# Optimization experiments

Hardware: AMD Instinct MI355X
Metric: run time of the kernel (lower is better)

The kernel has to match this reference:

```python
import jax, jax.numpy as jnp
from jax import lax
import numpy as np

N_LAYER = 2
SEQ, BATCH, D = 4096, 32, 512


def setup_inputs() -> dict:
    key = jax.random.key(0)
    k1, k2, k3 = jax.random.split(key, 3)
    x = jax.random.normal(k1, (SEQ, BATCH, D), dtype=jnp.float32)
    # repo init: weight_ih ~ N(0, 0.01)
    W_ih = jax.random.normal(k2, (N_LAYER, D, D), dtype=jnp.float32) * 0.01
    # recurrent weight in [0,1) keeps the long ReLU recurrence bounded
    w_hh = jax.random.uniform(k3, (N_LAYER, D), dtype=jnp.float32)
    b_ih = jnp.zeros((N_LAYER, D), dtype=jnp.float32)
    return {"x": x, "W_ih": W_ih, "w_hh": w_hh, "b_ih": b_ih}


def _indrnn_layer(x, W, w, b):
    # x: (T, B, in), W: (H, in), w,b: (H,)
    proj = jnp.einsum('tbi,hi->tbh', x, W) + b  # one batched GEMM up front

    def step(h, p):
        h = jax.nn.relu(p + w * h)
        return h, h

    h0 = jnp.zeros((x.shape[1], W.shape[0]), dtype=x.dtype)
    hT, ys = lax.scan(step, h0, proj)
    return ys, hT


def reference(x, W_ih, w_hh, b_ih):
    hiddens = []
    out = x
    for l in range(W_ih.shape[0]):  # small fixed layer loop
        out, hT = _indrnn_layer(out, W_ih[l], w_hh[l], b_ih[l])
        hiddens.append(hT)
    h_n = jnp.stack(hiddens, axis=0)  # (n_layer, B, H)
    return out, h_n
```

## Files before the change

kernel.cpp:

```cpp
#include <hip/hip_runtime.h>

#define T_SEQ   4096
#define BATCH   32
#define DIM     512
#define MROWS   (T_SEQ * BATCH)
#define S_STRIDE (BATCH * DIM)
#define OUT_ELEMS ((size_t)T_SEQ * BATCH * DIM)
#define NCH     32
#define CLEN    (T_SEQ / NCH)
#define NCHAIN  (BATCH * DIM)
#define NWG     ((MROWS / 128) * (DIM / 128))

typedef __bf16 bf8_t __attribute__((ext_vector_type(8)));
typedef float  f4_t  __attribute__((ext_vector_type(4)));
typedef unsigned short u16x8 __attribute__((ext_vector_type(8)));
typedef __attribute__((address_space(1))) void gvoid_t;
typedef __attribute__((address_space(3))) void lvoid_t;

__device__ __forceinline__ unsigned short f2bf(float f) {
    unsigned int u = __float_as_uint(f);
    u += 0x7FFFu + ((u >> 16) & 1u);
    return (unsigned short)(u >> 16);
}
__device__ __forceinline__ float bf2f(unsigned short b) {
    return __uint_as_float(((unsigned int)b) << 16);
}

__global__ __launch_bounds__(256) void k_cvt(const float* __restrict__ in,
                                             unsigned short* __restrict__ out) {
    size_t i = ((size_t)blockIdx.x * 256 + threadIdx.x) * 8;
    float4 a = *reinterpret_cast<const float4*>(in + i);
    float4 b = *reinterpret_cast<const float4*>(in + i + 4);
    u16x8 o;
    o[0] = f2bf(a.x); o[1] = f2bf(a.y); o[2] = f2bf(a.z); o[3] = f2bf(a.w);
    o[4] = f2bf(b.x); o[5] = f2bf(b.y); o[6] = f2bf(b.z); o[7] = f2bf(b.w);
    *reinterpret_cast<u16x8*>(out + i) = o;
}

template <int AF32>
__global__ __launch_bounds__(256)
void k_gemm_bt(const void* __restrict__ Ap,
               const unsigned short* __restrict__ B,
               unsigned short* __restrict__ C) {
    __shared__ unsigned short As[128 * 32];
    __shared__ unsigned short Bs[128 * 32];

    const int tid  = threadIdx.x;
    const int lane = tid & 63;
    const int wv   = tid >> 6;
    const int wr   = wv >> 1;
    const int wc   = wv & 1;

    const int flat = blockIdx.x;
    const int s    = (flat & 7) * (NWG / 8) + (flat >> 3);
    const size_t gm = (size_t)(s >> 2) * 128;
    const int    gn = (s & 3) * 128;

    const int srow = tid >> 2;
    const int skk  = (tid & 3) * 8;

    f4_t acc[4][4] = {};

    const int l15 = lane & 15;
    const int lk  = (lane >> 4) * 8;

    for (int k0 = 0; k0 < 512; k0 += 32) {
#pragma unroll
        for (int i = 0; i < 2; ++i) {
            const unsigned short* gb = B + (size_t)(gn + i * 64 + srow) * 512 + k0 + skk;
            __builtin_amdgcn_global_load_lds((gvoid_t*)gb, (lvoid_t*)&Bs[i * 2048 + wv * 512], 16, 0, 0);
            if constexpr (AF32) {
                const float* ga = (const float*)Ap + (gm + (size_t)(i * 64 + srow)) * 512 + k0 + skk;
                float4 a0 = *reinterpret_cast<const float4*>(ga);
                float4 a1 = *reinterpret_cast<const float4*>(ga + 4);
                u16x8 o;
                o[0] = f2bf(a0.x); o[1] = f2bf(a0.y); o[2] = f2bf(a0.z); o[3] = f2bf(a0.w);
                o[4] = f2bf(a1.x); o[5] = f2bf(a1.y); o[6] = f2bf(a1.z); o[7] = f2bf(a1.w);
                *reinterpret_cast<u16x8*>(&As[i * 2048 + tid * 8]) = o;
            } else {
                const unsigned short* ga = (const unsigned short*)Ap + (gm + (size_t)(i * 64 + srow)) * 512 + k0 + skk;
                __builtin_amdgcn_global_load_lds((gvoid_t*)ga, (lvoid_t*)&As[i * 2048 + wv * 512], 16, 0, 0);
            }
        }
        __syncthreads();

        bf8_t af[4], bfz[4];
#pragma unroll
        for (int m = 0; m < 4; ++m)
            af[m] = *reinterpret_cast<const bf8_t*>(&As[(wr * 64 + m * 16 + l15) * 32 + lk]);
#pragma unroll
        for (int n = 0; n < 4; ++n)
            bfz[n] = *reinterpret_cast<const bf8_t*>(&Bs[(wc * 64 + n * 16 + l15) * 32 + lk]);
#pragma unroll
        for (int m = 0; m < 4; ++m)
#pragma unroll
            for (int n = 0; n < 4; ++n)
                acc[m][n] = __builtin_amdgcn_mfma_f32_16x16x32_bf16(af[m], bfz[n], acc[m][n], 0, 0, 0);
        __syncthreads();
    }

    const int crow0 = (lane >> 4) * 4;
#pragma unroll
    for (int m = 0; m < 4; ++m)
#pragma unroll
        for (int n = 0; n < 4; ++n) {
            const size_t row0 = gm + (size_t)(wr * 64 + m * 16 + crow0);
            const int    col  = gn + wc * 64 + n * 16 + l15;
#pragma unroll
            for (int r = 0; r < 4; ++r)
                C[(row0 + r) * 512 + col] = f2bf(acc[m][n][r]);
        }
}

__global__ __launch_bounds__(256)
void k_scan_p1(const unsigned short* __restrict__ q,
               const float* __restrict__ w_hh,
               const float* __restrict__ b_ih,
               float* __restrict__ Asum,
               float* __restrict__ Bsum) {
    const int g = (blockIdx.x & 63) * 256 + threadIdx.x;
    const int c = blockIdx.x >> 6;
    const float w  = w_hh[g & 511];
    const float bs = b_ih[g & 511];
    const unsigned short* p = q + (size_t)c * CLEN * S_STRIDE + g;

    float A = 0.f, Bv = 0.f;
    float s0[8], s1[8];
#pragma unroll
    for (int j = 0; j < 8; ++j) s0[j] = bf2f(p[(size_t)j * S_STRIDE]);
#pragma unroll
    for (int j = 0; j < 8; ++j) s1[j] = bf2f(p[(size_t)(8 + j) * S_STRIDE]);

    for (int j0 = 0; j0 < CLEN; j0 += 16) {
#pragma unroll
        for (int j = 0; j < 8; ++j) {
            float qv = s0[j] + bs;
            A  = fmaxf(fmaf(w, A, qv), 0.f);
            Bv = fmaf(w, Bv, qv);
        }
        if (j0 + 16 < CLEN) {
#pragma unroll
            for (int j = 0; j < 8; ++j) s0[j] = bf2f(p[(size_t)(j0 + 16 + j) * S_STRIDE]);
        }
#pragma unroll
        for (int j = 0; j < 8; ++j) {
            float qv = s1[j] + bs;
            A  = fmaxf(fmaf(w, A, qv), 0.f);
            Bv = fmaf(w, Bv, qv);
        }
        if (j0 + 24 < CLEN) {
#pragma unroll
            for (int j = 0; j < 8; ++j) s1[j] = bf2f(p[(size_t)(j0 + 24 + j) * S_STRIDE]);
        }
    }
    Asum[(size_t)c * NCHAIN + g] = A;
    Bsum[(size_t)c * NCHAIN + g] = Bv;
}

template <int MODE>
__global__ __launch_bounds__(256)
void k_scan_p2(const unsigned short* __restrict__ q,
               const float* __restrict__ w_hh,
               const float* __restrict__ b_ih,
               const float* __restrict__ Asum,
               const float* __restrict__ Bsum,
               float* __restrict__ of32,
               unsigned short* __restrict__ ob16,
               float* __restrict__ hT) {
    const int g = (blockIdx.x & 63) * 256 + threadIdx.x;
    const int c = blockIdx.x >> 6;
    const float w  = w_hh[g & 511];
    const float bs = b_ih[g & 511];

    float cw = w;
#pragma unroll
    for (int i = 0; i < 7; ++i) cw *= cw;
    float h = 0.f;
    for (int cc = 0; cc < c; ++cc)
        h = fmaxf(Asum[(size_t)cc * NCHAIN + g], fmaf(cw, h, Bsum[(size_t)cc * NCHAIN + g]));

    const size_t base = (size_t)c * CLEN * S_STRIDE + g;
    const unsigned short* p = q + base;

    float s0[8], s1[8];
#pragma unroll
    for (int j = 0; j < 8; ++j) s0[j] = bf2f(p[(size_t)j * S_STRIDE]);
#pragma unroll
    for (int j = 0; j < 8; ++j) s1[j] = bf2f(p[(size_t)(8 + j) * S_STRIDE]);

    for (int j0 = 0; j0 < CLEN; j0 += 16) {
#pragma unroll
        for (int j = 0; j < 8; ++j) {
            h = fmaxf(fmaf(w, h, s0[j] + bs), 0.f);
            const size_t idx = base + (size_t)(j0 + j) * S_STRIDE;
            if (MODE == 0) of32[idx] = h; else ob16[idx] = f2bf(h);
        }
        if (j0 + 16 < CLEN) {
#pragma unroll
            for (int j = 0; j < 8; ++j) s0[j] = bf2f(p[(size_t)(j0 + 16 + j) * S_STRIDE]);
        }
#pragma unroll
        for (int j = 0; j < 8; ++j) {
            h = fmaxf(fmaf(w, h, s1[j] + bs), 0.f);
            const size_t idx = base + (size_t)(j0 + 8 + j) * S_STRIDE;
            if (MODE == 0) of32[idx] = h; else ob16[idx] = f2bf(h);
        }
        if (j0 + 24 < CLEN) {
#pragma unroll
            for (int j = 0; j < 8; ++j) s1[j] = bf2f(p[(size_t)(j0 + 24 + j) * S_STRIDE]);
        }
    }
    if (c == NCH - 1) hT[g] = h;
}

extern "C" void kernel_launch(void* const* d_in, const int* in_sizes, int n_in,
                              void* d_out, int out_size, void* d_ws, size_t ws_size,
                              hipStream_t stream) {
    const float* x    = (const float*)d_in[0];
    const float* W_ih = (const float*)d_in[1];
    const float* w_hh = (const float*)d_in[2];
    const float* b_ih = (const float*)d_in[3];

    unsigned short* proj2 = (unsigned short*)d_ws;
    unsigned short* Wb    = proj2 + OUT_ELEMS;
    float* Asum = (float*)(Wb + 2 * 512 * 512);
    float* Bsum = Asum + (size_t)NCH * NCHAIN;

    unsigned short* proj1 = (unsigned short*)d_out;
    unsigned short* ys1   = proj1 + OUT_ELEMS;
    float* out = (float*)d_out;
    float* hT  = out + OUT_ELEMS;

    const int sgrid = 64 * NCH;

    k_cvt<<<524288 / 8 / 256, 256, 0, stream>>>(W_ih, Wb);
    k_gemm_bt<1><<<NWG, 256, 0, stream>>>(x, Wb, proj1);
    k_scan_p1<<<sgrid, 256, 0, stream>>>(proj1, w_hh, b_ih, Asum, Bsum);
    k_scan_p2<1><<<sgrid, 256, 0, stream>>>(proj1, w_hh, b_ih, Asum, Bsum,
                                            nullptr, ys1, hT);
    k_gemm_bt<0><<<NWG, 256, 0, stream>>>(ys1, Wb + 512 * 512, proj2);
    k_scan_p1<<<sgrid, 256, 0, stream>>>(proj2, w_hh + DIM, b_ih + DIM, Asum, Bsum);
    k_scan_p2<0><<<sgrid, 256, 0, stream>>>(proj2, w_hh + DIM, b_ih + DIM, Asum, Bsum,
                                            out, nullptr, hT + NCHAIN);
}
```

Before: 469.1 us.

## Rewrite projection GEMM to keep full weight slice resident in LDS

The tiled GEMM, which staged both A and B through LDS in K-steps of 32 with two barriers per step, is replaced. Each workgroup now loads a full 128x512 weight slice (padded rows) into LDS once. Its eight waves then stream A rows straight from global memory into registers, with software-pipelined prefetch, across 2048 rows. This removes per-K-step barriers and A staging through LDS and reuses B across many row tiles. In exchange it uses about 130KB of dynamic LDS per block, direct uncoalesced-ish per-lane A loads, a 256-block grid, and heavy register pressure at 512 threads with a min-blocks-per-CU hint of 2.

```diff
diff --git a/kernel.cpp b/kernel.cpp
--- a/kernel.cpp
+++ b/kernel.cpp
@@ -9,13 +9,13 @@
 #define NCH     32
 #define CLEN    (T_SEQ / NCH)
 #define NCHAIN  (BATCH * DIM)
-#define NWG     ((MROWS / 128) * (DIM / 128))
+
+#define BROW    520
+#define LDS_BYTES (128 * BROW * 2)
 
 typedef __bf16 bf8_t __attribute__((ext_vector_type(8)));
 typedef float  f4_t  __attribute__((ext_vector_type(4)));
 typedef unsigned short u16x8 __attribute__((ext_vector_type(8)));
-typedef __attribute__((address_space(1))) void gvoid_t;
-typedef __attribute__((address_space(3))) void lvoid_t;
 
 __device__ __forceinline__ unsigned short f2bf(float f) {
     unsigned int u = __float_as_uint(f);
@@ -38,78 +38,102 @@
 }
 
 template <int AF32>
-__global__ __launch_bounds__(256)
-void k_gemm_bt(const void* __restrict__ Ap,
+__global__ __launch_bounds__(512, 2)
+void k_gemm_rs(const void* __restrict__ Ap,
                const unsigned short* __restrict__ B,
                unsigned short* __restrict__ C) {
-    __shared__ unsigned short As[128 * 32];
-    __shared__ unsigned short Bs[128 * 32];
+    extern __shared__ unsigned short Bs[];
 
     const int tid  = threadIdx.x;
     const int lane = tid & 63;
-    const int wv   = tid >> 6;
-    const int wr   = wv >> 1;
-    const int wc   = wv & 1;
-
-    const int flat = blockIdx.x;
-    const int s    = (flat & 7) * (NWG / 8) + (flat >> 3);
-    const size_t gm = (size_t)(s >> 2) * 128;
-    const int    gn = (s & 3) * 128;
-
-    const int srow = tid >> 2;
-    const int skk  = (tid & 3) * 8;
-
-    f4_t acc[4][4] = {};
-
-    const int l15 = lane & 15;
-    const int lk  = (lane >> 4) * 8;
-
-    for (int k0 = 0; k0 < 512; k0 += 32) {
-#pragma unroll
-        for (int i = 0; i < 2; ++i) {
-            const unsigned short* gb = B + (size_t)(gn + i * 64 + srow) * 512 + k0 + skk;
-            __builtin_amdgcn_global_load_lds((gvoid_t*)gb, (lvoid_t*)&Bs[i * 2048 + wv * 512], 16, 0, 0);
-            if constexpr (AF32) {
-                const float* ga = (const float*)Ap + (gm + (size_t)(i * 64 + srow)) * 512 + k0 + skk;
-                float4 a0 = *reinterpret_cast<const float4*>(ga);
-                float4 a1 = *reinterpret_cast<const float4*>(ga + 4);
-                u16x8 o;
-                o[0] = f2bf(a0.x); o[1] = f2bf(a0.y); o[2] = f2bf(a0.z); o[3] = f2bf(a0.w);
-                o[4] = f2bf(a1.x); o[5] = f2bf(a1.y); o[6] = f2bf(a1.z); o[7] = f2bf(a1.w);
-                *reinterpret_cast<u16x8*>(&As[i * 2048 + tid * 8]) = o;
-            } else {
-                const unsigned short* ga = (const unsigned short*)Ap + (gm + (size_t)(i * 64 + srow)) * 512 + k0 + skk;
-                __builtin_amdgcn_global_load_lds((gvoid_t*)ga, (lvoid_t*)&As[i * 2048 + wv * 512], 16, 0, 0);
+    const int w    = tid >> 6;
+    const int l15  = lane & 15;
+    const int lk   = (lane >> 4) * 8;
+    const int n_t  = blockIdx.x >> 6;
+    const int mg   = blockIdx.x & 63;
+    const int gn   = n_t * 128;
+
+    {
+        const int lc = tid >> 2, s0 = tid & 3;
+        const unsigned short* gB = B + (size_t)(gn + lc) * 512;
+#pragma unroll
+        for (int j = 0; j < 16; ++j) {
+            const int seg = j * 4 + s0;
+            u16x8 v = *reinterpret_cast<const u16x8*>(gB + seg * 8);
+            *reinterpret_cast<u16x8*>(&Bs[lc * BROW + seg * 8]) = v;
+        }
+    }
+    __syncthreads();
+
+    const int bbase = l15 * BROW + lk;
+
+    for (int ms = 0; ms < 8; ++ms) {
+        const size_t R0 = (size_t)mg * 2048 + ms * 256 + w * 32;
+        f4_t acc[2][8] = {};
+
+        const unsigned short* arp[2];
+        const float*          afp[2];
+#pragma unroll
+        for (int m = 0; m < 2; ++m) {
+            if constexpr (AF32) afp[m] = (const float*)Ap + (R0 + m * 16 + l15) * 512;
+            else                arp[m] = (const unsigned short*)Ap + (R0 + m * 16 + l15) * 512;
+        }
+
+        bf8_t a0[2], a1[2], a2[2], b0[8], b1[8];
+
+#define LOAD_A(dst, k0)                                                        \
+        _Pragma("unroll")                                                      \
+        for (int m = 0; m < 2; ++m) {                                          \
+            if constexpr (AF32) {                                              \
+                float4 f0 = *reinterpret_cast<const float4*>(afp[m] + (k0) + lk);     \
+                float4 f1 = *reinterpret_cast<const float4*>(afp[m] + (k0) + lk + 4); \
+                u16x8 o;                                                       \
+                o[0] = f2bf(f0.x); o[1] = f2bf(f0.y); o[2] = f2bf(f0.z); o[3] = f2bf(f0.w); \
+                o[4] = f2bf(f1.x); o[5] = f2bf(f1.y); o[6] = f2bf(f1.z); o[7] = f2bf(f1.w); \
+                dst[m] = *reinterpret_cast<bf8_t*>(&o);                        \
+            } else {                                                           \
+                dst[m] = *reinterpret_cast<const bf8_t*>(arp[m] + (k0) + lk);  \
+            }                                                                  \
+        }
+#define LOAD_B(dst, k0)                                                        \
+        _Pragma("unroll")                                                      \
+        for (int n = 0; n < 8; ++n)                                            \
+            dst[n] = *reinterpret_cast<const bf8_t*>(&Bs[bbase + n * 16 * BROW + (k0)]);
+
+        LOAD_A(a0, 0)
+        LOAD_A(a1, 32)
+        LOAD_B(b0, 0)
+
+#pragma unroll
+        for (int ks = 0; ks < 16; ++ks) {
+            const int k0 = ks * 32;
+            if (ks < 14) { LOAD_A(a2, k0 + 64) }
+            if (ks < 15) { LOAD_B(b1, k0 + 32) }
+#pragma unroll
+            for (int m = 0; m < 2; ++m)
+#pragma unroll
+                for (int n = 0; n < 8; ++n)
+                    acc[m][n] = __builtin_amdgcn_mfma_f32_16x16x32_bf16(a0[m], b0[n], acc[m][n], 0, 0, 0);
+#pragma unroll
+            for (int m = 0; m < 2; ++m) { a0[m] = a1[m]; a1[m] = a2[m]; }
+#pragma unroll
+            for (int n = 0; n < 8; ++n) b0[n] = b1[n];
+        }
+#undef LOAD_A
+#undef LOAD_B
+
+        const int crow0 = (lane >> 4) * 4;
+#pragma unroll
+        for (int m = 0; m < 2; ++m)
+#pragma unroll
+            for (int n = 0; n < 8; ++n) {
+                const size_t row0 = R0 + m * 16 + crow0;
+                const int    col  = gn + n * 16 + l15;
+#pragma unroll
+                for (int r = 0; r < 4; ++r)
+                    C[(row0 + r) * 512 + col] = f2bf(acc[m][n][r]);
             }
-        }
-        __syncthreads();
-
-        bf8_t af[4], bfz[4];
-#pragma unroll
-        for (int m = 0; m < 4; ++m)
-            af[m] = *reinterpret_cast<const bf8_t*>(&As[(wr * 64 + m * 16 + l15) * 32 + lk]);
-#pragma unroll
-        for (int n = 0; n < 4; ++n)
-            bfz[n] = *reinterpret_cast<const bf8_t*>(&Bs[(wc * 64 + n * 16 + l15) * 32 + lk]);
-#pragma unroll
-        for (int m = 0; m < 4; ++m)
-#pragma unroll
-            for (int n = 0; n < 4; ++n)
-                acc[m][n] = __builtin_amdgcn_mfma_f32_16x16x32_bf16(af[m], bfz[n], acc[m][n], 0, 0, 0);
-        __syncthreads();
-    }
-
-    const int crow0 = (lane >> 4) * 4;
-#pragma unroll
-    for (int m = 0; m < 4; ++m)
-#pragma unroll
-        for (int n = 0; n < 4; ++n) {
-            const size_t row0 = gm + (size_t)(wr * 64 + m * 16 + crow0);
-            const int    col  = gn + wc * 64 + n * 16 + l15;
-#pragma unroll
-            for (int r = 0; r < 4; ++r)
-                C[(row0 + r) * 512 + col] = f2bf(acc[m][n][r]);
-        }
+    }
 }
 
 __global__ __launch_bounds__(256)
@@ -234,11 +258,11 @@
     const int sgrid = 64 * NCH;
 
     k_cvt<<<524288 / 8 / 256, 256, 0, stream>>>(W_ih, Wb);
-    k_gemm_bt<1><<<NWG, 256, 0, stream>>>(x, Wb, proj1);
+    k_gemm_rs<1><<<256, 512, LDS_BYTES, stream>>>(x, Wb, proj1);
     k_scan_p1<<<sgrid, 256, 0, stream>>>(proj1, w_hh, b_ih, Asum, Bsum);
     k_scan_p2<1><<<sgrid, 256, 0, stream>>>(proj1, w_hh, b_ih, Asum, Bsum,
                                             nullptr, ys1, hT);
-    k_gemm_bt<0><<<NWG, 256, 0, stream>>>(ys1, Wb + 512 * 512, proj2);
+    k_gemm_rs<0><<<256, 512, LDS_BYTES, stream>>>(ys1, Wb + 512 * 512, proj2);
     k_scan_p1<<<sgrid, 256, 0, stream>>>(proj2, w_hh + DIM, b_ih + DIM, Asum, Bsum);
     k_scan_p2<0><<<sgrid, 256, 0, stream>>>(proj2, w_hh + DIM, b_ih + DIM, Asum, Bsum,
                                             out, nullptr, hT + NCHAIN);
```

Result: slower. 1.139 ms (+142.9%).

## Double-buffer LDS tiles in bf16 GEMM to overlap loads with MFMA

Applied to the files above, without the earlier changes.

Splits the GEMM's LDS A/B tiles into two buffers and prefetches the next K-slice (async global_load_lds for bf16, register-staged float loads for the f32 A path) while MFMAs run on the current slice. This drops one __syncthreads per K-iteration and is meant to hide global memory latency behind compute. In exchange it doubles LDS use per workgroup, which may reduce occupancy, and the f32 path holds extra registers for the staged loads.

```diff
diff --git a/kernel.cpp b/kernel.cpp
--- a/kernel.cpp
+++ b/kernel.cpp
@@ -42,8 +42,8 @@
 void k_gemm_bt(const void* __restrict__ Ap,
                const unsigned short* __restrict__ B,
                unsigned short* __restrict__ C) {
-    __shared__ unsigned short As[128 * 32];
-    __shared__ unsigned short Bs[128 * 32];
+    __shared__ unsigned short As[2][128 * 32];
+    __shared__ unsigned short Bs[2][128 * 32];
 
     const int tid  = threadIdx.x;
     const int lane = tid & 63;
@@ -60,44 +60,77 @@
     const int skk  = (tid & 3) * 8;
 
     f4_t acc[4][4] = {};
-
     const int l15 = lane & 15;
     const int lk  = (lane >> 4) * 8;
 
-    for (int k0 = 0; k0 < 512; k0 += 32) {
-#pragma unroll
-        for (int i = 0; i < 2; ++i) {
-            const unsigned short* gb = B + (size_t)(gn + i * 64 + srow) * 512 + k0 + skk;
-            __builtin_amdgcn_global_load_lds((gvoid_t*)gb, (lvoid_t*)&Bs[i * 2048 + wv * 512], 16, 0, 0);
-            if constexpr (AF32) {
-                const float* ga = (const float*)Ap + (gm + (size_t)(i * 64 + srow)) * 512 + k0 + skk;
-                float4 a0 = *reinterpret_cast<const float4*>(ga);
-                float4 a1 = *reinterpret_cast<const float4*>(ga + 4);
-                u16x8 o;
-                o[0] = f2bf(a0.x); o[1] = f2bf(a0.y); o[2] = f2bf(a0.z); o[3] = f2bf(a0.w);
-                o[4] = f2bf(a1.x); o[5] = f2bf(a1.y); o[6] = f2bf(a1.z); o[7] = f2bf(a1.w);
-                *reinterpret_cast<u16x8*>(&As[i * 2048 + tid * 8]) = o;
-            } else {
-                const unsigned short* ga = (const unsigned short*)Ap + (gm + (size_t)(i * 64 + srow)) * 512 + k0 + skk;
-                __builtin_amdgcn_global_load_lds((gvoid_t*)ga, (lvoid_t*)&As[i * 2048 + wv * 512], 16, 0, 0);
-            }
-        }
-        __syncthreads();
+    float4 fa0[2], fa1[2];
+
+#define ISSUE_A_F32(k0)                                                        \
+    _Pragma("unroll")                                                          \
+    for (int i = 0; i < 2; ++i) {                                              \
+        const float* ga = (const float*)Ap + (gm + (size_t)(i * 64 + srow)) * 512 + (k0) + skk; \
+        fa0[i] = *reinterpret_cast<const float4*>(ga);                         \
+        fa1[i] = *reinterpret_cast<const float4*>(ga + 4);                     \
+    }
+#define WRITE_A_F32(b)                                                         \
+    _Pragma("unroll")                                                          \
+    for (int i = 0; i < 2; ++i) {                                              \
+        u16x8 o;                                                               \
+        o[0] = f2bf(fa0[i].x); o[1] = f2bf(fa0[i].y); o[2] = f2bf(fa0[i].z); o[3] = f2bf(fa0[i].w); \
+        o[4] = f2bf(fa1[i].x); o[5] = f2bf(fa1[i].y); o[6] = f2bf(fa1[i].z); o[7] = f2bf(fa1[i].w); \
+        *reinterpret_cast<u16x8*>(&As[b][i * 2048 + tid * 8]) = o;             \
+    }
+#define GLL_A(b, k0)                                                           \
+    _Pragma("unroll")                                                          \
+    for (int i = 0; i < 2; ++i) {                                              \
+        const unsigned short* ga = (const unsigned short*)Ap + (gm + (size_t)(i * 64 + srow)) * 512 + (k0) + skk; \
+        __builtin_amdgcn_global_load_lds((gvoid_t*)ga, (lvoid_t*)&As[b][i * 2048 + wv * 512], 16, 0, 0); \
+    }
+#define GLL_B(b, k0)                                                           \
+    _Pragma("unroll")                                                          \
+    for (int i = 0; i < 2; ++i) {                                              \
+        const unsigned short* gb = B + (size_t)(gn + i * 64 + srow) * 512 + (k0) + skk; \
+        __builtin_amdgcn_global_load_lds((gvoid_t*)gb, (lvoid_t*)&Bs[b][i * 2048 + wv * 512], 16, 0, 0); \
+    }
+
+    if constexpr (AF32) { ISSUE_A_F32(0) } else { GLL_A(0, 0) }
+    GLL_B(0, 0)
+    if constexpr (AF32) { WRITE_A_F32(0) }
+    __syncthreads();
+
+#pragma unroll 2
+    for (int ks = 0; ks < 16; ++ks) {
+        const int cur = ks & 1;
+        const int nxt = cur ^ 1;
+        const int k1  = (ks + 1) * 32;
+
+        if (ks < 15) {
+            if constexpr (AF32) { ISSUE_A_F32(k1) } else { GLL_A(nxt, k1) }
+            GLL_B(nxt, k1)
+        }
 
         bf8_t af[4], bfz[4];
 #pragma unroll
         for (int m = 0; m < 4; ++m)
-            af[m] = *reinterpret_cast<const bf8_t*>(&As[(wr * 64 + m * 16 + l15) * 32 + lk]);
+            af[m] = *reinterpret_cast<const bf8_t*>(&As[cur][(wr * 64 + m * 16 + l15) * 32 + lk]);
 #pragma unroll
         for (int n = 0; n < 4; ++n)
-            bfz[n] = *reinterpret_cast<const bf8_t*>(&Bs[(wc * 64 + n * 16 + l15) * 32 + lk]);
+            bfz[n] = *reinterpret_cast<const bf8_t*>(&Bs[cur][(wc * 64 + n * 16 + l15) * 32 + lk]);
 #pragma unroll
         for (int m = 0; m < 4; ++m)
 #pragma unroll
             for (int n = 0; n < 4; ++n)
                 acc[m][n] = __builtin_amdgcn_mfma_f32_16x16x32_bf16(af[m], bfz[n], acc[m][n], 0, 0, 0);
+
+        if (ks < 15) {
+            if constexpr (AF32) { WRITE_A_F32(nxt) }
+        }
         __syncthreads();
     }
+#undef ISSUE_A_F32
+#undef WRITE_A_F32
+#undef GLL_A
+#undef GLL_B
 
     const int crow0 = (lane >> 4) * 4;
 #pragma unroll
```

Measured after the change: 465.8 us. No clear change (-0.7%).

## Rewrite projection GEMM as 256x256 double-buffered 8-wave pipelined kernel

Applied to the files above, without the earlier changes.

Replaces the 128x128, 4-wave, single-buffered GEMM with a 256x256-tile, 8-wave kernel. It uses a 64-wide K step, double-buffered LDS with an XOR swizzle, and explicit waitcnt/barrier/setprio phases so global loads overlap MFMA work. For the fp32 input layer, the A tile is prefetched into registers and converted to bf16 while the previous tile computes. The cost is about 128KB of dynamic LDS per block and far fewer workgroups. This lowers occupancy, and the hand-counted vmcnt scheduling can break silently if the load counts change.

```diff
diff --git a/kernel.cpp b/kernel.cpp
--- a/kernel.cpp
+++ b/kernel.cpp
@@ -9,7 +9,13 @@
 #define NCH     32
 #define CLEN    (T_SEQ / NCH)
 #define NCHAIN  (BATCH * DIM)
-#define NWG     ((MROWS / 128) * (DIM / 128))
+
+#define GNWG    ((MROWS / 256) * (DIM / 256))
+#define OFF_A0  0
+#define OFF_A1  16384
+#define OFF_B0  32768
+#define OFF_B1  49152
+#define GLDS_B  131072
 
 typedef __bf16 bf8_t __attribute__((ext_vector_type(8)));
 typedef float  f4_t  __attribute__((ext_vector_type(4)));
@@ -25,6 +31,15 @@
 __device__ __forceinline__ float bf2f(unsigned short b) {
     return __uint_as_float(((unsigned int)b) << 16);
 }
+
+#define VMC(n)  asm volatile("s_waitcnt vmcnt(" #n ")" ::: "memory")
+#define LGKM0   asm volatile("s_waitcnt lgkmcnt(0)" ::: "memory")
+#define PH_PRE()  do { __builtin_amdgcn_s_barrier(); LGKM0;                    \
+                       __builtin_amdgcn_sched_barrier(0);                      \
+                       __builtin_amdgcn_s_setprio(1); } while (0)
+#define PH_POST() do { __builtin_amdgcn_s_setprio(0);                          \
+                       __builtin_amdgcn_sched_barrier(0);                      \
+                       __builtin_amdgcn_s_barrier(); } while (0)
 
 __global__ __launch_bounds__(256) void k_cvt(const float* __restrict__ in,
                                              unsigned short* __restrict__ out) {
@@ -38,73 +53,177 @@
 }
 
 template <int AF32>
-__global__ __launch_bounds__(256)
-void k_gemm_bt(const void* __restrict__ Ap,
-               const unsigned short* __restrict__ B,
-               unsigned short* __restrict__ C) {
-    __shared__ unsigned short As[128 * 32];
-    __shared__ unsigned short Bs[128 * 32];
+__global__ __launch_bounds__(512, 2)
+void k_gemm8(const void* __restrict__ Ap,
+             const unsigned short* __restrict__ Bp,
+             unsigned short* __restrict__ C) {
+    extern __shared__ unsigned short lds[];
 
     const int tid  = threadIdx.x;
     const int lane = tid & 63;
     const int wv   = tid >> 6;
-    const int wr   = wv >> 1;
-    const int wc   = wv & 1;
-
-    const int flat = blockIdx.x;
-    const int s    = (flat & 7) * (NWG / 8) + (flat >> 3);
-    const size_t gm = (size_t)(s >> 2) * 128;
-    const int    gn = (s & 3) * 128;
-
-    const int srow = tid >> 2;
-    const int skk  = (tid & 3) * 8;
-
-    f4_t acc[4][4] = {};
-
-    const int l15 = lane & 15;
-    const int lk  = (lane >> 4) * 8;
-
-    for (int k0 = 0; k0 < 512; k0 += 32) {
-#pragma unroll
-        for (int i = 0; i < 2; ++i) {
-            const unsigned short* gb = B + (size_t)(gn + i * 64 + srow) * 512 + k0 + skk;
-            __builtin_amdgcn_global_load_lds((gvoid_t*)gb, (lvoid_t*)&Bs[i * 2048 + wv * 512], 16, 0, 0);
-            if constexpr (AF32) {
-                const float* ga = (const float*)Ap + (gm + (size_t)(i * 64 + srow)) * 512 + k0 + skk;
-                float4 a0 = *reinterpret_cast<const float4*>(ga);
-                float4 a1 = *reinterpret_cast<const float4*>(ga + 4);
-                u16x8 o;
-                o[0] = f2bf(a0.x); o[1] = f2bf(a0.y); o[2] = f2bf(a0.z); o[3] = f2bf(a0.w);
-                o[4] = f2bf(a1.x); o[5] = f2bf(a1.y); o[6] = f2bf(a1.z); o[7] = f2bf(a1.w);
-                *reinterpret_cast<u16x8*>(&As[i * 2048 + tid * 8]) = o;
-            } else {
-                const unsigned short* ga = (const unsigned short*)Ap + (gm + (size_t)(i * 64 + srow)) * 512 + k0 + skk;
-                __builtin_amdgcn_global_load_lds((gvoid_t*)ga, (lvoid_t*)&As[i * 2048 + wv * 512], 16, 0, 0);
+    const int wr   = wv >> 2;
+    const int wc   = wv & 3;
+    const int l15  = lane & 15;
+    const int l16  = lane >> 4;
+    const int lj   = lane >> 3;
+    const int ss8  = lane & 7;
+
+    const int sid = (blockIdx.x & 7) * (GNWG / 8) + (blockIdx.x >> 3);
+    const size_t gm = (size_t)(sid >> 1) * 256;
+    const int    gn = (sid & 1) * 256;
+
+    const unsigned short* Ab = (const unsigned short*)Ap;
+    const float*          Af = (const float*)Ap;
+
+    auto stage = [&](const unsigned short* gbase, size_t grow0, int region,
+                     int half, int kt) {
+#pragma unroll
+        for (int j = 0; j < 2; ++j) {
+            const int r = half * 128 + j * 64 + wv * 8 + lj;
+            const unsigned short* src =
+                gbase + (grow0 + r) * 512 + kt * 64 + ((ss8 ^ (r & 7)) * 8);
+            unsigned short* dst = &lds[region + half * 8192 + j * 4096 + wv * 512];
+            __builtin_amdgcn_global_load_lds((gvoid_t*)src, (lvoid_t*)dst, 16, 0, 0);
+        }
+    };
+    auto loadAf = [&](float4* h, int half, int kt) {
+#pragma unroll
+        for (int j = 0; j < 2; ++j) {
+            const int r = half * 128 + j * 64 + wv * 8 + lj;
+            const float* src = Af + (gm + r) * 512 + kt * 64 + ss8 * 8;
+            h[j * 2]     = *reinterpret_cast<const float4*>(src);
+            h[j * 2 + 1] = *reinterpret_cast<const float4*>(src + 4);
+        }
+    };
+    auto writeAf = [&](const float4* h, int region, int half) {
+#pragma unroll
+        for (int j = 0; j < 2; ++j) {
+            const int r = half * 128 + j * 64 + wv * 8 + lj;
+            float4 f0 = h[j * 2], f1 = h[j * 2 + 1];
+            u16x8 o;
+            o[0] = f2bf(f0.x); o[1] = f2bf(f0.y); o[2] = f2bf(f0.z); o[3] = f2bf(f0.w);
+            o[4] = f2bf(f1.x); o[5] = f2bf(f1.y); o[6] = f2bf(f1.z); o[7] = f2bf(f1.w);
+            *reinterpret_cast<u16x8*>(&lds[region + r * 64 + (ss8 ^ (r & 7)) * 8]) = o;
+        }
+    };
+
+    f4_t  acc[8][4] = {};
+    bf8_t bb[4][2];
+    bf8_t aq[2][2];
+    float4 afh0[4], afh1[4];
+
+    auto loadBall = [&](int region) {
+#pragma unroll
+        for (int n = 0; n < 4; ++n)
+#pragma unroll
+            for (int ks = 0; ks < 2; ++ks) {
+                const int c  = wc * 64 + n * 16 + l15;
+                const int sl = (ks * 4 + l16) ^ (l15 & 7);
+                bb[n][ks] = *reinterpret_cast<const bf8_t*>(
+                    (const char*)&lds[region] + c * 128 + sl * 16);
             }
-        }
-        __syncthreads();
-
-        bf8_t af[4], bfz[4];
-#pragma unroll
-        for (int m = 0; m < 4; ++m)
-            af[m] = *reinterpret_cast<const bf8_t*>(&As[(wr * 64 + m * 16 + l15) * 32 + lk]);
-#pragma unroll
-        for (int n = 0; n < 4; ++n)
-            bfz[n] = *reinterpret_cast<const bf8_t*>(&Bs[(wc * 64 + n * 16 + l15) * 32 + lk]);
-#pragma unroll
-        for (int m = 0; m < 4; ++m)
-#pragma unroll
-            for (int n = 0; n < 4; ++n)
-                acc[m][n] = __builtin_amdgcn_mfma_f32_16x16x32_bf16(af[m], bfz[n], acc[m][n], 0, 0, 0);
-        __syncthreads();
+    };
+    auto loadAq = [&](int region, int q) {
+#pragma unroll
+        for (int m = 0; m < 2; ++m)
+#pragma unroll
+            for (int ks = 0; ks < 2; ++ks) {
+                const int r  = wr * 128 + (q * 2 + m) * 16 + l15;
+                const int sl = (ks * 4 + l16) ^ (l15 & 7);
+                aq[m][ks] = *reinterpret_cast<const bf8_t*>(
+                    (const char*)&lds[region] + r * 128 + sl * 16);
+            }
+    };
+#define MFMA_Q(q)                                                              \
+    _Pragma("unroll")                                                          \
+    for (int m = 0; m < 2; ++m)                                                \
+        _Pragma("unroll")                                                      \
+        for (int n = 0; n < 4; ++n)                                            \
+            _Pragma("unroll")                                                  \
+            for (int ks = 0; ks < 2; ++ks)                                     \
+                acc[(q) * 2 + m][n] = __builtin_amdgcn_mfma_f32_16x16x32_bf16( \
+                    aq[m][ks], bb[n][ks], acc[(q) * 2 + m][n], 0, 0, 0);
+
+    if constexpr (AF32) {
+        loadAf(afh0, 0, 0); loadAf(afh1, 1, 0);
+        stage(Bp, (size_t)gn, OFF_B0, 0, 0); stage(Bp, (size_t)gn, OFF_B0, 1, 0);
+        stage(Bp, (size_t)gn, OFF_B1, 0, 1); stage(Bp, (size_t)gn, OFF_B1, 1, 1);
+        VMC(8);
+        writeAf(afh0, OFF_A0, 0); writeAf(afh1, OFF_A0, 1);
+        VMC(4);
+        LGKM0;
+    } else {
+        stage(Ab, gm, OFF_A0, 0, 0); stage(Ab, gm, OFF_A0, 1, 0);
+        stage(Bp, (size_t)gn, OFF_B0, 0, 0); stage(Bp, (size_t)gn, OFF_B0, 1, 0);
+        stage(Bp, (size_t)gn, OFF_B1, 0, 1); stage(Bp, (size_t)gn, OFF_B1, 1, 1);
+        VMC(4);
     }
-
-    const int crow0 = (lane >> 4) * 4;
-#pragma unroll
-    for (int m = 0; m < 4; ++m)
+    __builtin_amdgcn_s_barrier();
+
+#pragma unroll
+    for (int i = 0; i < 4; ++i) {
+        const int t1 = 2 * i + 1, t2 = 2 * i + 2, t3 = 2 * i + 3;
+        const bool st2 = (i < 3);
+
+        loadBall(OFF_B0); loadAq(OFF_A0, 0);
+        if constexpr (AF32) { loadAf(afh0, 0, t1); } else { stage(Ab, gm, OFF_A1, 0, t1); }
+        PH_PRE(); MFMA_Q(0); PH_POST();
+        loadAq(OFF_A0, 1);
+        if constexpr (AF32) { loadAf(afh1, 1, t1); } else { stage(Ab, gm, OFF_A1, 1, t1); }
+        PH_PRE(); MFMA_Q(1); PH_POST();
+        loadAq(OFF_A0, 2);
+        if (st2) stage(Bp, (size_t)gn, OFF_B0, 0, t2);
+        PH_PRE(); MFMA_Q(2);
+        __builtin_amdgcn_s_setprio(0); __builtin_amdgcn_sched_barrier(0);
+        if constexpr (AF32) {
+            if (st2) { VMC(6); } else { VMC(4); }
+            writeAf(afh0, OFF_A1, 0);
+        }
+        __builtin_amdgcn_s_barrier();
+        loadAq(OFF_A0, 3);
+        if (st2) stage(Bp, (size_t)gn, OFF_B0, 1, t2);
+        PH_PRE(); MFMA_Q(3);
+        __builtin_amdgcn_s_setprio(0); __builtin_amdgcn_sched_barrier(0);
+        if constexpr (AF32) {
+            if (st2) { VMC(4); } else { VMC(0); }
+            writeAf(afh1, OFF_A1, 1);
+            LGKM0;
+        } else {
+            if (st2) { VMC(4); } else { VMC(0); }
+        }
+        __builtin_amdgcn_s_barrier();
+
+        loadBall(OFF_B1); loadAq(OFF_A1, 0);
+        if (st2) { if constexpr (AF32) { loadAf(afh0, 0, t2); } else { stage(Ab, gm, OFF_A0, 0, t2); } }
+        PH_PRE(); MFMA_Q(0); PH_POST();
+        loadAq(OFF_A1, 1);
+        if (st2) { if constexpr (AF32) { loadAf(afh1, 1, t2); } else { stage(Ab, gm, OFF_A0, 1, t2); } }
+        PH_PRE(); MFMA_Q(1); PH_POST();
+        loadAq(OFF_A1, 2);
+        if (st2) stage(Bp, (size_t)gn, OFF_B1, 0, t3);
+        PH_PRE(); MFMA_Q(2);
+        __builtin_amdgcn_s_setprio(0); __builtin_amdgcn_sched_barrier(0);
+        if constexpr (AF32) { if (st2) { VMC(6); writeAf(afh0, OFF_A0, 0); } }
+        __builtin_amdgcn_s_barrier();
+        loadAq(OFF_A1, 3);
+        if (st2) stage(Bp, (size_t)gn, OFF_B1, 1, t3);
+        PH_PRE(); MFMA_Q(3);
+        __builtin_amdgcn_s_setprio(0); __builtin_amdgcn_sched_barrier(0);
+        if (st2) {
+            VMC(4);
+            if constexpr (AF32) { writeAf(afh1, OFF_A0, 1); LGKM0; }
+        }
+        __builtin_amdgcn_s_barrier();
+    }
+#undef MFMA_Q
+
+    const int crow0 = l16 * 4;
+#pragma unroll
+    for (int m = 0; m < 8; ++m)
 #pragma unroll
         for (int n = 0; n < 4; ++n) {
-            const size_t row0 = gm + (size_t)(wr * 64 + m * 16 + crow0);
+            const size_t row0 = gm + (size_t)(wr * 128 + m * 16 + crow0);
             const int    col  = gn + wc * 64 + n * 16 + l15;
 #pragma unroll
             for (int r = 0; r < 4; ++r)
@@ -221,6 +340,11 @@
     const float* w_hh = (const float*)d_in[2];
     const float* b_ih = (const float*)d_in[3];
 
+    hipFuncSetAttribute(reinterpret_cast<const void*>(&k_gemm8<1>),
+                        hipFuncAttributeMaxDynamicSharedMemorySize, GLDS_B);
+    hipFuncSetAttribute(reinterpret_cast<const void*>(&k_gemm8<0>),
+                        hipFuncAttributeMaxDynamicSharedMemorySize, GLDS_B);
+
     unsigned short* proj2 = (unsigned short*)d_ws;
     unsigned short* Wb    = proj2 + OUT_ELEMS;
     float* Asum = (float*)(Wb + 2 * 512 * 512);
@@ -234,11 +358,11 @@
     const int sgrid = 64 * NCH;
 
     k_cvt<<<524288 / 8 / 256, 256, 0, stream>>>(W_ih, Wb);
-    k_gemm_bt<1><<<NWG, 256, 0, stream>>>(x, Wb, proj1);
+    k_gemm8<1><<<GNWG, 512, GLDS_B, stream>>>(x, Wb, proj1);
     k_scan_p1<<<sgrid, 256, 0, stream>>>(proj1, w_hh, b_ih, Asum, Bsum);
     k_scan_p2<1><<<sgrid, 256, 0, stream>>>(proj1, w_hh, b_ih, Asum, Bsum,
                                             nullptr, ys1, hT);
-    k_gemm_bt<0><<<NWG, 256, 0, stream>>>(ys1, Wb + 512 * 512, proj2);
+    k_gemm8<0><<<GNWG, 512, GLDS_B, stream>>>(ys1, Wb + 512 * 512, proj2);
     k_scan_p1<<<sgrid, 256, 0, stream>>>(proj2, w_hh + DIM, b_ih + DIM, Asum, Bsum);
     k_scan_p2<0><<<sgrid, 256, 0, stream>>>(proj2, w_hh + DIM, b_ih + DIM, Asum, Bsum,
                                             out, nullptr, hT + NCHAIN);
```

After: 406.2 us, median of 2. 1.15x faster.
